# Optimization experiments

Hardware: AMD Instinct MI355X
Metric: run time of the kernel (lower is better)

The kernel has to match this reference:

```python
import jax, jax.numpy as jnp
import numpy as np

L, Q = 200, 21          # alignment length, number of Potts states (20 AAs + gap)
REG_H, REG_J = 0.01, 0.01  # L2 regularization strengths (reg_h, reg_J)
M = 1024                # number of sequences in the MSA


def setup_inputs() -> dict:
    key = jax.random.key(0)
    ks = jax.random.split(key, 6)
    X_tokens = jax.random.randint(ks[0], (M, L), 0, Q)
    weights = jax.random.uniform(ks[1], (M,), dtype=jnp.float32)
    fi = jax.random.uniform(ks[2], (L, Q), dtype=jnp.float32)
    fi_target = fi / fi.sum(axis=1, keepdims=True)  # single-site frequencies
    fij = jax.random.uniform(ks[3], (L, Q, L, Q), dtype=jnp.float32)
    fij_target = fij / fij.sum(axis=(1, 3), keepdims=True)  # pairwise frequencies
    h = jax.random.normal(ks[4], (L, Q), dtype=jnp.float32) * 1e-4
    J = jax.random.normal(ks[5], (L, Q, L, Q), dtype=jnp.float32) * 1e-4
    # remove_autocorr: zero self-couplings J[i,:,i,:]
    eye = jnp.eye(L, dtype=jnp.float32)[:, None, :, None]
    J = J * (1.0 - eye)
    return {"X_tokens": X_tokens, "weights": weights, "fi_target": fi_target,
            "fij_target": fij_target, "h": h, "J": J}


def _loss_third(X, weights, fi_target, fij_target, h, J):
    # loss_third_fn: sites i in [2L//3, L)
    start = 2 * L // 3
    w = weights / weights.sum()
    sites = jnp.arange(start, L)                         # (S,)
    causal = (jnp.arange(L)[None, :] < sites[:, None])   # (S, L), j < i mask
    Jm = J[start:] * causal[:, None, :, None].astype(J.dtype)  # (S, q, L, q)
    # energy_i = fi[i] @ h[i] + sum_{j<i} J[i,:,j,:] * fij[i,:,j,:], summed over i
    energy = (jnp.einsum('ia,ia->', fi_target[start:], h[start:])
              + jnp.einsum('iajb,iajb->', Jm, fij_target[start:]))
    # logits[n,i,a] = h[i,a] + sum_{j<i,b} J[i,a,j,b] * X[n,j,b]
    logits = jnp.einsum('njb,iajb->nia', X, Jm) + h[start:][None]  # (M, S, q)
    logZ = jax.scipy.special.logsumexp(logits, axis=-1)            # (M, S)
    nll = -(energy - jnp.einsum('ni,n->', logZ, w))
    loss = nll + REG_H * jnp.sum(h * h) + REG_J * jnp.sum(J * J)
    return loss, nll


def reference(X_tokens, weights, fi_target, fij_target, h, J):
    X = jax.nn.one_hot(X_tokens, Q, dtype=jnp.float32)  # (M, L, q)
    return _loss_third(X, weights, fi_target, fij_target, h, J)
```

## Files before the change

### kernel.cpp

```cpp
#include <hip/hip_runtime.h>
#include <cstdint>

#define LL    200
#define QQ    21
#define MM    1024
#define START 133
#define NS    67
#define RGH   0.01f
#define RGJ   0.01f

#define SLOT_J2  0
#define SLOT_E   64
#define SLOT_LZ  128
#define TOKT_OFF 1024
#define TOKT_BYTES ((size_t)LL * MM * 4)
#define SLAB_OFF (TOKT_OFF + TOKT_BYTES)
#define SLAB_BYTES ((size_t)2 * NS * QQ * MM * 4)
#define WS_FULL (SLAB_OFF + SLAB_BYTES)
#define WS_TOK  SLAB_OFF

#define TJ 12
#define PLANE 256
#define TILE_FLOATS (QQ * PLANE)

typedef const uint32_t __attribute__((address_space(1)))* gq_t;
typedef uint32_t __attribute__((address_space(3)))* lq_t;

__device__ __forceinline__ float block_reduce_sum_256(float v) {
  __shared__ float sm[4];
  #pragma unroll
  for (int off = 32; off > 0; off >>= 1) v += __shfl_down(v, off, 64);
  const int lane = threadIdx.x & 63;
  const int wv   = threadIdx.x >> 6;
  __syncthreads();
  if (lane == 0) sm[wv] = v;
  __syncthreads();
  float r = 0.0f;
  if (threadIdx.x == 0) r = sm[0] + sm[1] + sm[2] + sm[3];
  return r;
}

__device__ __forceinline__ void dma_tile(
    const float* __restrict__ Ji, int j0, int rem, int wv, int lane,
    float* __restrict__ tile) {
  const int nlanes = (rem * QQ + 3) >> 2;
  if (lane < nlanes) {
    for (int a = wv; a < QQ; a += 4) {
      const float* g = Ji + a * (LL * QQ) + j0 * QQ + lane * 4;
      __builtin_amdgcn_global_load_lds((gq_t)g, (lq_t)(tile + a * PLANE),
                                       16, 0, 0);
    }
  }
}

__device__ __forceinline__ void tok_load(
    const int* __restrict__ tokT, const int* __restrict__ Xtok, int useT,
    int j0, int jend, int n, int (&bo)[TJ]) {
  #pragma unroll
  for (int k = 0; k < TJ; ++k) {
    if (j0 + k < jend) {
      const int j = j0 + k;
      const int b = useT ? tokT[j * MM + n] : Xtok[n * LL + j];
      bo[k] = k * QQ + b;
    }
  }
}

__device__ __forceinline__ void gather_tile(
    const float* __restrict__ tile, const int (&bo)[TJ], int rem,
    float (&lg)[QQ]) {
  #pragma unroll
  for (int jl = 0; jl < TJ; ++jl) {
    if (jl >= rem) break;
    const float* p = tile + bo[jl];
    #pragma unroll
    for (int a = 0; a < QQ; ++a) lg[a] += p[a * PLANE];
  }
}

template <bool MONO>
__device__ __forceinline__ void logz_body(
    const float* __restrict__ J, const int* __restrict__ tokT,
    const int* __restrict__ Xtok, int useT, const float* __restrict__ h,
    const float* __restrict__ w, float* __restrict__ slab,
    float* __restrict__ acc, float (*lds)[TILE_FLOATS]) {
  const int iI = blockIdx.x;
  const int i  = START + iI;
  const int y  = MONO ? 0 : blockIdx.y;
  const int h0 = i >> 1;
  const int jbeg = MONO ? 0 : (y ? h0 : 0);
  const int jend = MONO ? i : (y ? i : h0);
  const int t = threadIdx.x, lane = t & 63, wv = t >> 6;
  const int n = blockIdx.z * 256 + t;
  const float* Ji = J + (size_t)i * (QQ * LL * QQ);
  const int ntiles = (jend - jbeg + TJ - 1) / TJ;

  float lg[QQ];
  #pragma unroll
  for (int a = 0; a < QQ; ++a) lg[a] = 0.0f;
  int boc[TJ], bon[TJ];

  dma_tile(Ji, jbeg, min(TJ, jend - jbeg), wv, lane, lds[0]);
  tok_load(tokT, Xtok, useT, jbeg, jend, n, boc);
  __syncthreads();

  for (int s = 0; s < ntiles; ++s) {
    const int j0  = jbeg + s * TJ;
    const int rem = min(TJ, jend - j0);
    const bool more = (s + 1 < ntiles);
    if (more) {
      const int j1 = j0 + TJ;
      dma_tile(Ji, j1, min(TJ, jend - j1), wv, lane, lds[(s + 1) & 1]);
      tok_load(tokT, Xtok, useT, j1, jend, n, bon);
    }
    gather_tile(lds[s & 1], boc, rem, lg);
    if (more) {
      #pragma unroll
      for (int k = 0; k < TJ; ++k) boc[k] = bon[k];
    }
    __syncthreads();
  }

  if (MONO) {
    const float* hi = h + i * QQ;
    float mx = -3.0e38f;
    #pragma unroll
    for (int a = 0; a < QQ; ++a) { lg[a] += hi[a]; mx = fmaxf(mx, lg[a]); }
    float sme = 0.0f;
    #pragma unroll
    for (int a = 0; a < QQ; ++a) sme += expf(lg[a] - mx);
    const float contrib = w[n] * (mx + logf(sme));
    const float tot = block_reduce_sum_256(contrib);
    if (t == 0) atomicAdd(acc + SLOT_LZ + (blockIdx.x & 63), tot);
  } else {
    float* dst = slab + (((size_t)y * NS + iI) * QQ) * MM + n;
    #pragma unroll
    for (int a = 0; a < QQ; ++a) dst[a * MM] = lg[a];
  }
}

__global__ __launch_bounds__(256) void kern_logz_p1(
    const float* __restrict__ J, const int* __restrict__ tokT,
    float* __restrict__ slab) {
  __shared__ float lds[2][TILE_FLOATS];
  logz_body<false>(J, tokT, nullptr, 1, nullptr, nullptr, slab, nullptr, lds);
}

__global__ __launch_bounds__(256) void kern_logz_mono(
    const float* __restrict__ J, const int* __restrict__ tokT,
    const int* __restrict__ Xtok, int useT, const float* __restrict__ h,
    const float* __restrict__ w, float* __restrict__ acc) {
  __shared__ float lds[2][TILE_FLOATS];
  logz_body<true>(J, tokT, Xtok, useT, h, w, nullptr, acc, lds);
}

__global__ __launch_bounds__(128) void kern_logz_p2(
    const float* __restrict__ slab, const float* __restrict__ h,
    const float* __restrict__ w, float* __restrict__ acc) {
  const int iI = blockIdx.x;
  const int n  = blockIdx.y * 128 + threadIdx.x;
  const float* s0 = slab + ((size_t)iI * QQ) * MM + n;
  const float* s1 = slab + (((size_t)NS + iI) * QQ) * MM + n;
  const float* hi = h + (START + iI) * QQ;
  float lg[QQ];
  float mx = -3.0e38f;
  #pragma unroll
  for (int a = 0; a < QQ; ++a) {
    lg[a] = s0[a * MM] + s1[a * MM] + hi[a];
    mx = fmaxf(mx, lg[a]);
  }
  float sme = 0.0f;
  #pragma unroll
  for (int a = 0; a < QQ; ++a) sme += expf(lg[a] - mx);
  float v = w[n] * (mx + logf(sme));
  #pragma unroll
  for (int off = 32; off > 0; off >>= 1) v += __shfl_down(v, off, 64);
  __shared__ float sm[2];
  if ((threadIdx.x & 63) == 0) sm[threadIdx.x >> 6] = v;
  __syncthreads();
  if (threadIdx.x == 0)
    atomicAdd(acc + SLOT_LZ + (blockIdx.x & 63), sm[0] + sm[1]);
}

__global__ __launch_bounds__(256) void kern_jsum(
    const float* __restrict__ J, const float* __restrict__ fij,
    float* __restrict__ acc) {
  const int t = threadIdx.x;
  const float4* __restrict__ J4 = (const float4*)J;
  float j2 = 0.0f;
  for (int f = blockIdx.x * 256 + t; f < (LL * QQ * LL * QQ / 4);
       f += 1024 * 256) {
    const float4 v = J4[f];
    j2 += v.x * v.x + v.y * v.y + v.z * v.z + v.w * v.w;
  }
  float e = 0.0f;
  for (int r = blockIdx.x; r < NS * QQ; r += 1024) {
    const int iI = r / QQ;
    const int a  = r - iI * QQ;
    const int i  = START + iI;
    const size_t base = (size_t)i * (QQ * LL * QQ) + (size_t)a * (LL * QQ);
    const float4* __restrict__ Jb = (const float4*)(J + base);
    const float4* __restrict__ Fb = (const float4*)(fij + base);
    const int lim  = i * QQ;
    const int lim4 = lim >> 2;
    for (int f = t; f < lim4; f += 256) {
      const float4 v = Jb[f], u = Fb[f];
      e += v.x * u.x + v.y * u.y + v.z * u.z + v.w * u.w;
    }
    const int rem = lim & 3;
    if (t < rem) {
      const int p = lim4 * 4 + t;
      e += (J + base)[p] * (fij + base)[p];
    }
  }
  const float tj2 = block_reduce_sum_256(j2);
  const float te  = block_reduce_sum_256(e);
  if (t == 0) {
    atomicAdd(acc + SLOT_J2 + (blockIdx.x & 63), tj2);
    atomicAdd(acc + SLOT_E  + (blockIdx.x & 63), te);
  }
}

__global__ __launch_bounds__(256) void kern_tokT(
    const int* __restrict__ X, int* __restrict__ tokT) {
  const int idx = blockIdx.x * 256 + threadIdx.x;
  if (idx < LL * MM) {
    const int j = idx / MM;
    const int n = idx - j * MM;
    tokT[idx] = X[n * LL + j];
  }
}

__global__ __launch_bounds__(256) void kern_final(
    const float* __restrict__ h, const float* __restrict__ fi,
    const float* __restrict__ w, const float* __restrict__ acc,
    float* __restrict__ out) {
  const int t = threadIdx.x;
  const float sj2 = block_reduce_sum_256(t < 64 ? acc[SLOT_J2 + t] : 0.0f);
  const float se  = block_reduce_sum_256(t < 64 ? acc[SLOT_E + t] : 0.0f);
  const float slz = block_reduce_sum_256(t < 64 ? acc[SLOT_LZ + t] : 0.0f);
  float hs = 0.0f, eh = 0.0f, ws = 0.0f;
  for (int idx = t; idx < LL * QQ; idx += 256) {
    const float hv = h[idx];
    hs += hv * hv;
    if (idx >= START * QQ) eh += fi[idx] * hv;
  }
  for (int idx = t; idx < MM; idx += 256) ws += w[idx];
  const float ths = block_reduce_sum_256(hs);
  const float teh = block_reduce_sum_256(eh);
  const float tws = block_reduce_sum_256(ws);
  if (t == 0) {
    const float energy = teh + se;
    const float nll = slz / tws - energy;
    out[0] = nll + RGH * ths + RGJ * sj2;
    out[1] = nll;
  }
}

extern "C" void kernel_launch(void* const* d_in, const int* in_sizes, int n_in,
                              void* d_out, int out_size, void* d_ws, size_t ws_size,
                              hipStream_t stream) {
  const int*   Xtok = (const int*)  d_in[0];
  const float* wts  = (const float*)d_in[1];
  const float* fi   = (const float*)d_in[2];
  const float* fij  = (const float*)d_in[3];
  const float* h    = (const float*)d_in[4];
  const float* J    = (const float*)d_in[5];
  float* out  = (float*)d_out;
  float* acc  = (float*)d_ws;
  int*   tokT = (int*)((char*)d_ws + TOKT_OFF);
  float* slab = (float*)((char*)d_ws + SLAB_OFF);

  hipMemsetAsync(d_ws, 0, 1024, stream);
  if (ws_size >= WS_FULL) {
    kern_tokT<<<(LL * MM + 255) / 256, 256, 0, stream>>>(Xtok, tokT);
    kern_jsum<<<1024, 256, 0, stream>>>(J, fij, acc);
    kern_logz_p1<<<dim3(NS, 2, 4), 256, 0, stream>>>(J, tokT, slab);
    kern_logz_p2<<<dim3(NS, 8), 128, 0, stream>>>(slab, h, wts, acc);
    kern_final<<<1, 256, 0, stream>>>(h, fi, wts, acc, out);
  } else if (ws_size >= WS_TOK) {
    kern_tokT<<<(LL * MM + 255) / 256, 256, 0, stream>>>(Xtok, tokT);
    kern_jsum<<<1024, 256, 0, stream>>>(J, fij, acc);
    kern_logz_mono<<<dim3(NS, 1, 4), 256, 0, stream>>>(J, tokT, Xtok, 1, h, wts, acc);
    kern_final<<<1, 256, 0, stream>>>(h, fi, wts, acc, out);
  } else {
    kern_jsum<<<1024, 256, 0, stream>>>(J, fij, acc);
    kern_logz_mono<<<dim3(NS, 1, 4), 256, 0, stream>>>(J, nullptr, Xtok, 0, h, wts, acc);
    kern_final<<<1, 256, 0, stream>>>(h, fi, wts, acc, out);
  }
}
```

Before: 218.6 us.

## Merge J-sum and logZ phase-1 into one horizontally fused launch

Combines the J-squared/energy reduction kernel and the logZ partial-logit kernel into a single grid. Low block indices run the logZ tiles and the rest run the J-sum streaming, so the two independent phases overlap on the GPU instead of running back to back. The logZ blocks are placed first so the longer-latency tiles start early. All blocks now reserve the double-buffered LDS tile, including the J-sum blocks that never use it, which may lower occupancy for the streaming part.

New measurement: 207.0 us. -5.3%, faster.

```diff
diff --git a/kernel.cpp b/kernel.cpp
--- a/kernel.cpp
+++ b/kernel.cpp
@@ -23,6 +23,9 @@
 #define PLANE 256
 #define TILE_FLOATS (QQ * PLANE)
 
+#define NB_P1 (NS * 8)
+#define NB_JS 1024
+
 typedef const uint32_t __attribute__((address_space(1)))* gq_t;
 typedef uint32_t __attribute__((address_space(3)))* lq_t;
 
@@ -83,15 +86,14 @@
     const float* __restrict__ J, const int* __restrict__ tokT,
     const int* __restrict__ Xtok, int useT, const float* __restrict__ h,
     const float* __restrict__ w, float* __restrict__ slab,
-    float* __restrict__ acc, float (*lds)[TILE_FLOATS]) {
-  const int iI = blockIdx.x;
+    float* __restrict__ acc, int iI, int y, int z,
+    float (*lds)[TILE_FLOATS]) {
   const int i  = START + iI;
-  const int y  = MONO ? 0 : blockIdx.y;
   const int h0 = i >> 1;
   const int jbeg = MONO ? 0 : (y ? h0 : 0);
   const int jend = MONO ? i : (y ? i : h0);
   const int t = threadIdx.x, lane = t & 63, wv = t >> 6;
-  const int n = blockIdx.z * 256 + t;
+  const int n = z * 256 + t;
   const float* Ji = J + (size_t)i * (QQ * LL * QQ);
   const int ntiles = (jend - jbeg + TJ - 1) / TJ;
 
@@ -131,7 +133,7 @@
     for (int a = 0; a < QQ; ++a) sme += expf(lg[a] - mx);
     const float contrib = w[n] * (mx + logf(sme));
     const float tot = block_reduce_sum_256(contrib);
-    if (t == 0) atomicAdd(acc + SLOT_LZ + (blockIdx.x & 63), tot);
+    if (t == 0) atomicAdd(acc + SLOT_LZ + (iI & 63), tot);
   } else {
     float* dst = slab + (((size_t)y * NS + iI) * QQ) * MM + n;
     #pragma unroll
@@ -139,62 +141,18 @@
   }
 }
 
-__global__ __launch_bounds__(256) void kern_logz_p1(
-    const float* __restrict__ J, const int* __restrict__ tokT,
-    float* __restrict__ slab) {
-  __shared__ float lds[2][TILE_FLOATS];
-  logz_body<false>(J, tokT, nullptr, 1, nullptr, nullptr, slab, nullptr, lds);
-}
-
-__global__ __launch_bounds__(256) void kern_logz_mono(
-    const float* __restrict__ J, const int* __restrict__ tokT,
-    const int* __restrict__ Xtok, int useT, const float* __restrict__ h,
-    const float* __restrict__ w, float* __restrict__ acc) {
-  __shared__ float lds[2][TILE_FLOATS];
-  logz_body<true>(J, tokT, Xtok, useT, h, w, nullptr, acc, lds);
-}
-
-__global__ __launch_bounds__(128) void kern_logz_p2(
-    const float* __restrict__ slab, const float* __restrict__ h,
-    const float* __restrict__ w, float* __restrict__ acc) {
-  const int iI = blockIdx.x;
-  const int n  = blockIdx.y * 128 + threadIdx.x;
-  const float* s0 = slab + ((size_t)iI * QQ) * MM + n;
-  const float* s1 = slab + (((size_t)NS + iI) * QQ) * MM + n;
-  const float* hi = h + (START + iI) * QQ;
-  float lg[QQ];
-  float mx = -3.0e38f;
-  #pragma unroll
-  for (int a = 0; a < QQ; ++a) {
-    lg[a] = s0[a * MM] + s1[a * MM] + hi[a];
-    mx = fmaxf(mx, lg[a]);
-  }
-  float sme = 0.0f;
-  #pragma unroll
-  for (int a = 0; a < QQ; ++a) sme += expf(lg[a] - mx);
-  float v = w[n] * (mx + logf(sme));
-  #pragma unroll
-  for (int off = 32; off > 0; off >>= 1) v += __shfl_down(v, off, 64);
-  __shared__ float sm[2];
-  if ((threadIdx.x & 63) == 0) sm[threadIdx.x >> 6] = v;
-  __syncthreads();
-  if (threadIdx.x == 0)
-    atomicAdd(acc + SLOT_LZ + (blockIdx.x & 63), sm[0] + sm[1]);
-}
-
-__global__ __launch_bounds__(256) void kern_jsum(
+__device__ __forceinline__ void jsum_body(
     const float* __restrict__ J, const float* __restrict__ fij,
-    float* __restrict__ acc) {
+    float* __restrict__ acc, int jb) {
   const int t = threadIdx.x;
   const float4* __restrict__ J4 = (const float4*)J;
   float j2 = 0.0f;
-  for (int f = blockIdx.x * 256 + t; f < (LL * QQ * LL * QQ / 4);
-       f += 1024 * 256) {
+  for (int f = jb * 256 + t; f < (LL * QQ * LL * QQ / 4); f += NB_JS * 256) {
     const float4 v = J4[f];
     j2 += v.x * v.x + v.y * v.y + v.z * v.z + v.w * v.w;
   }
   float e = 0.0f;
-  for (int r = blockIdx.x; r < NS * QQ; r += 1024) {
+  for (int r = jb; r < NS * QQ; r += NB_JS) {
     const int iI = r / QQ;
     const int a  = r - iI * QQ;
     const int i  = START + iI;
@@ -216,9 +174,68 @@
   const float tj2 = block_reduce_sum_256(j2);
   const float te  = block_reduce_sum_256(e);
   if (t == 0) {
-    atomicAdd(acc + SLOT_J2 + (blockIdx.x & 63), tj2);
-    atomicAdd(acc + SLOT_E  + (blockIdx.x & 63), te);
-  }
+    atomicAdd(acc + SLOT_J2 + (jb & 63), tj2);
+    atomicAdd(acc + SLOT_E  + (jb & 63), te);
+  }
+}
+
+__global__ __launch_bounds__(256) void kern_mega(
+    const float* __restrict__ J, const float* __restrict__ fij,
+    const int* __restrict__ tokT, float* __restrict__ slab,
+    float* __restrict__ acc) {
+  __shared__ float lds[2][TILE_FLOATS];
+  const int bx = blockIdx.x;
+  if (bx < NB_P1) {
+    const int iI  = bx % NS;
+    const int sub = bx / NS;
+    logz_body<false>(J, tokT, nullptr, 1, nullptr, nullptr, slab, acc,
+                     iI, sub & 1, sub >> 1, lds);
+  } else {
+    jsum_body(J, fij, acc, bx - NB_P1);
+  }
+}
+
+__global__ __launch_bounds__(256) void kern_logz_mono(
+    const float* __restrict__ J, const int* __restrict__ tokT,
+    const int* __restrict__ Xtok, int useT, const float* __restrict__ h,
+    const float* __restrict__ w, float* __restrict__ acc) {
+  __shared__ float lds[2][TILE_FLOATS];
+  logz_body<true>(J, tokT, Xtok, useT, h, w, nullptr, acc,
+                  blockIdx.x, 0, blockIdx.z, lds);
+}
+
+__global__ __launch_bounds__(256) void kern_jsum(
+    const float* __restrict__ J, const float* __restrict__ fij,
+    float* __restrict__ acc) {
+  jsum_body(J, fij, acc, blockIdx.x);
+}
+
+__global__ __launch_bounds__(128) void kern_logz_p2(
+    const float* __restrict__ slab, const float* __restrict__ h,
+    const float* __restrict__ w, float* __restrict__ acc) {
+  const int iI = blockIdx.x;
+  const int n  = blockIdx.y * 128 + threadIdx.x;
+  const float* s0 = slab + ((size_t)iI * QQ) * MM + n;
+  const float* s1 = slab + (((size_t)NS + iI) * QQ) * MM + n;
+  const float* hi = h + (START + iI) * QQ;
+  float lg[QQ];
+  float mx = -3.0e38f;
+  #pragma unroll
+  for (int a = 0; a < QQ; ++a) {
+    lg[a] = s0[a * MM] + s1[a * MM] + hi[a];
+    mx = fmaxf(mx, lg[a]);
+  }
+  float sme = 0.0f;
+  #pragma unroll
+  for (int a = 0; a < QQ; ++a) sme += expf(lg[a] - mx);
+  float v = w[n] * (mx + logf(sme));
+  #pragma unroll
+  for (int off = 32; off > 0; off >>= 1) v += __shfl_down(v, off, 64);
+  __shared__ float sm[2];
+  if ((threadIdx.x & 63) == 0) sm[threadIdx.x >> 6] = v;
+  __syncthreads();
+  if (threadIdx.x == 0)
+    atomicAdd(acc + SLOT_LZ + (blockIdx.x & 63), sm[0] + sm[1]);
 }
 
 __global__ __launch_bounds__(256) void kern_tokT(
@@ -274,17 +291,16 @@
   hipMemsetAsync(d_ws, 0, 1024, stream);
   if (ws_size >= WS_FULL) {
     kern_tokT<<<(LL * MM + 255) / 256, 256, 0, stream>>>(Xtok, tokT);
-    kern_jsum<<<1024, 256, 0, stream>>>(J, fij, acc);
-    kern_logz_p1<<<dim3(NS, 2, 4), 256, 0, stream>>>(J, tokT, slab);
+    kern_mega<<<NB_P1 + NB_JS, 256, 0, stream>>>(J, fij, tokT, slab, acc);
     kern_logz_p2<<<dim3(NS, 8), 128, 0, stream>>>(slab, h, wts, acc);
     kern_final<<<1, 256, 0, stream>>>(h, fi, wts, acc, out);
   } else if (ws_size >= WS_TOK) {
     kern_tokT<<<(LL * MM + 255) / 256, 256, 0, stream>>>(Xtok, tokT);
-    kern_jsum<<<1024, 256, 0, stream>>>(J, fij, acc);
+    kern_jsum<<<NB_JS, 256, 0, stream>>>(J, fij, acc);
     kern_logz_mono<<<dim3(NS, 1, 4), 256, 0, stream>>>(J, tokT, Xtok, 1, h, wts, acc);
     kern_final<<<1, 256, 0, stream>>>(h, fi, wts, acc, out);
   } else {
-    kern_jsum<<<1024, 256, 0, stream>>>(J, fij, acc);
+    kern_jsum<<<NB_JS, 256, 0, stream>>>(J, fij, acc);
     kern_logz_mono<<<dim3(NS, 1, 4), 256, 0, stream>>>(J, nullptr, Xtok, 0, h, wts, acc);
     kern_final<<<1, 256, 0, stream>>>(h, fi, wts, acc, out);
   }
```
